# Kernel tuning notes

Measured on AMD Instinct MI355X. Metric: run time of the kernel, lower is better.

Reference implementation:

```python
import jax, jax.numpy as jnp
import numpy as np

D_MODEL = 2048
NUM_Q_HEADS = 16
NUM_KV_HEADS = 4
HEAD_DIM = D_MODEL // NUM_Q_HEADS  # 128
NUM_GROUPS = NUM_Q_HEADS // NUM_KV_HEADS  # 4
ROPE_BASE = 10000.0


def _rope_cos_sin(seq_len, head_dim):
    inv_freq = 1.0 / (ROPE_BASE ** (jnp.arange(0, head_dim, 2, dtype=jnp.float32) / head_dim))
    t = jnp.arange(seq_len, dtype=jnp.float32)
    freqs = jnp.outer(t, inv_freq)            # [S, head_dim/2]
    emb = jnp.concatenate([freqs, freqs], -1)  # [S, head_dim]
    return jnp.cos(emb)[None, :, None, :], jnp.sin(emb)[None, :, None, :]


def _rotate_half(x):
    half = x.shape[-1] // 2
    return jnp.concatenate([-x[..., half:], x[..., :half]], axis=-1)


def setup_inputs() -> dict:
    key = jax.random.key(0)
    k0, k1, k2, k3, k4 = jax.random.split(key, 5)
    B, S = 2, 2048
    kv_dim = HEAD_DIM * NUM_KV_HEADS
    scale = D_MODEL ** -0.5
    return {
        "x": jax.random.normal(k0, (B, S, D_MODEL), jnp.float32),
        "attention_mask": jnp.ones((B, S), jnp.int32),
        "Wq": jax.random.normal(k1, (D_MODEL, D_MODEL), jnp.float32) * scale,
        "Wk": jax.random.normal(k2, (D_MODEL, kv_dim), jnp.float32) * scale,
        "Wv": jax.random.normal(k3, (D_MODEL, kv_dim), jnp.float32) * scale,
        "Wo": jax.random.normal(k4, (D_MODEL, D_MODEL), jnp.float32) * scale,
    }


def reference(x, attention_mask, Wq, Wk, Wv, Wo):
    B, S, _ = x.shape
    q = (x @ Wq).reshape(B, S, NUM_Q_HEADS, HEAD_DIM)
    k = (x @ Wk).reshape(B, S, NUM_KV_HEADS, HEAD_DIM)
    v = (x @ Wv).reshape(B, S, NUM_KV_HEADS, HEAD_DIM)

    cos, sin = _rope_cos_sin(S, HEAD_DIM)  # [1,S,1,hd]
    q = q * cos + _rotate_half(q) * sin
    k = k * cos + _rotate_half(k) * sin

    # [B, H, S, hd]; replicate KV heads across groups (repeat_interleave)
    q = q.transpose(0, 2, 1, 3)
    k = jnp.repeat(k.transpose(0, 2, 1, 3), NUM_GROUPS, axis=1)
    v = jnp.repeat(v.transpose(0, 2, 1, 3), NUM_GROUPS, axis=1)

    scale = HEAD_DIM ** -0.5
    scores = jnp.einsum("bhqd,bhkd->bhqk", q, k) * scale
    mask = attention_mask[:, None, None, :]  # [B,1,1,S] over keys
    scores = jnp.where(mask == 0, jnp.float32(-jnp.inf), scores)
    probs = jax.nn.softmax(scores, axis=-1)
    out = jnp.einsum("bhqk,bhkd->bhqd", probs, v)
    out = out.transpose(0, 2, 1, 3).reshape(B, S, D_MODEL)
    return out @ Wo
```

## Files before the change

### kernel.cpp

```cpp
#include <hip/hip_runtime.h>
#include <hip/hip_bf16.h>

typedef __attribute__((ext_vector_type(4))) float f32x4;
typedef __attribute__((ext_vector_type(16))) float f32x16;
typedef __attribute__((ext_vector_type(8))) short s16x8;
typedef __attribute__((ext_vector_type(4))) short s16x4;
typedef __attribute__((ext_vector_type(2))) unsigned int u32x2;

__device__ __forceinline__ float fexp2(float x) {
    float y; asm("v_exp_f32 %0, %1" : "=v"(y) : "v"(x)); return y;
}

__global__ void tables_prep(float* __restrict__ cosT2, float* __restrict__ sinT2,
                            const int* __restrict__ mask, float* __restrict__ mb) {
    const int bid = blockIdx.x;
    if (bid < 64) {
        const int j = bid;
        const float inv = exp2f(-(float)j * (13.287712379549449f / 64.f));
#pragma unroll
        for (int k = 0; k < 8; ++k) {
            const int s = k * 256 + threadIdx.x;
            const float f = (float)s * inv;
            cosT2[j * 2048 + s] = cosf(f);
            sinT2[j * 2048 + s] = sinf(f);
        }
    } else {
        const int idx = (bid - 64) * 256 + threadIdx.x;
        mb[idx] = (mask[idx] == 0) ? -1e30f : 0.f;
    }
}

__global__ __launch_bounds__(256)
void cast_f32_bf16(const float* __restrict__ src, __hip_bfloat16* __restrict__ dst, int n4) {
    const int i = blockIdx.x * 256 + threadIdx.x;
    if (i < n4) {
        f32x4 v = *reinterpret_cast<const f32x4*>(src + (size_t)i * 4);
        union { s16x4 v4; __hip_bfloat16 h[4]; } u;
#pragma unroll
        for (int j = 0; j < 4; ++j) u.h[j] = __float2bfloat16(v[j]);
        *reinterpret_cast<s16x4*>(dst + (size_t)i * 4) = u.v4;
    }
}

__global__ __launch_bounds__(256)
void transpose_cast_all(const float* __restrict__ Wq, const float* __restrict__ Wk,
                        const float* __restrict__ Wv, const float* __restrict__ Wo,
                        __hip_bfloat16* __restrict__ wqkv_t, __hip_bfloat16* __restrict__ wo_t) {
    __shared__ __align__(16) float t[32][33];
    const int tx = threadIdx.x, ty = threadIdx.y;
    const int xseg = blockIdx.x;
    const int r0 = blockIdx.y * 32;
    const float* src; __hip_bfloat16* dst; int C, c0; bool perm;
    if (xseg < 64)      { src = Wq; dst = wqkv_t;                  C = 2048; c0 = xseg * 32;        perm = true; }
    else if (xseg < 80) { src = Wk; dst = wqkv_t + 2048ULL * 2048; C = 512;  c0 = (xseg - 64) * 32; perm = true; }
    else if (xseg < 96) { src = Wv; dst = wqkv_t + 2560ULL * 2048; C = 512;  c0 = (xseg - 80) * 32; perm = false; }
    else                { src = Wo; dst = wo_t;                    C = 2048; c0 = (xseg - 96) * 32; perm = false; }
#pragma unroll
    for (int i = 0; i < 32; i += 8)
        t[ty + i][tx] = src[(size_t)(r0 + ty + i) * C + c0 + tx];
    __syncthreads();
#pragma unroll
    for (int i = 0; i < 32; i += 8) {
        int row = c0 + ty + i;
        if (perm)
            row = (row & ~127) + (row & 15) + 32 * ((row >> 4) & 3) + 16 * ((row >> 6) & 1);
        dst[(size_t)row * 2048 + r0 + tx] = __float2bfloat16(t[tx][ty + i]);
    }
}

__global__ __launch_bounds__(512, 1)
void gemm_qkv_fused(const __hip_bfloat16* __restrict__ A,
                    const __hip_bfloat16* __restrict__ Bt,
                    const float* __restrict__ cosT2, const float* __restrict__ sinT2,
                    __hip_bfloat16* __restrict__ Qr, __hip_bfloat16* __restrict__ Kr,
                    __hip_bfloat16* __restrict__ Vt, int K) {
    __shared__ __align__(16) __hip_bfloat16 sm[4][2][8192];
    const int tid = threadIdx.x;
    const int l = tid & 63, w = tid >> 6;
    const int lo = l & 15, hi = l >> 4;
    const int wm = w >> 2, wn = w & 3;
    const int id = blockIdx.x, slot = id >> 3;
    const int by = (id & 7) * 2 + slot / 12;
    const int bx = slot % 12;
    const int row0 = by * 256;
    const int col0 = bx * 256;
    const int nk = K >> 5;

    f32x4 acc[8][4];
#pragma unroll
    for (int mi = 0; mi < 8; ++mi)
#pragma unroll
        for (int ni = 0; ni < 4; ++ni) acc[mi][ni] = f32x4{0.f, 0.f, 0.f, 0.f};

    auto ldlds = [&](const __hip_bfloat16* gsrc, __hip_bfloat16* ldst) {
        __builtin_amdgcn_global_load_lds(
            (const __attribute__((address_space(1))) void*)gsrc,
            (__attribute__((address_space(3))) void*)ldst, 16, 0, 0);
    };
    auto stage = [&](int kt) {
        const int s = kt & 3, k0 = kt << 5;
#pragma unroll
        for (int i = 0; i < 2; ++i) {
            const int c = i * 512 + tid;
            const int r = c >> 2, sw = ((c & 3) ^ ((r >> 1) & 3)) * 8;
            ldlds(A + (size_t)(row0 + r) * K + k0 + sw, &sm[s][0][c * 8]);
        }
#pragma unroll
        for (int i = 0; i < 2; ++i) {
            const int c = i * 512 + tid;
            const int r = c >> 2, sw = ((c & 3) ^ ((r >> 1) & 3)) * 8;
            ldlds(Bt + (size_t)(col0 + r) * K + k0 + sw, &sm[s][1][c * 8]);
        }
    };

    stage(0); stage(1); stage(2);
    for (int kt = 0; kt < nk; ++kt) {
        const int s = kt & 3;
        if (kt < nk - 2)       asm volatile("s_waitcnt vmcnt(8)" ::: "memory");
        else if (kt == nk - 2) asm volatile("s_waitcnt vmcnt(4)" ::: "memory");
        else                   asm volatile("s_waitcnt vmcnt(0)" ::: "memory");
        asm volatile("s_waitcnt lgkmcnt(0)" ::: "memory");
        asm volatile("s_barrier" ::: "memory");
        if (kt + 3 < nk) stage(kt + 3);

        s16x8 af[8], bf[4];
        const int rsw = ((lo >> 1) & 3);
#pragma unroll
        for (int mi = 0; mi < 8; ++mi)
            af[mi] = *reinterpret_cast<const s16x8*>(
                &sm[s][0][(wm * 128 + mi * 16 + lo) * 32 + ((hi ^ rsw) * 8)]);
#pragma unroll
        for (int ni = 0; ni < 4; ++ni)
            bf[ni] = *reinterpret_cast<const s16x8*>(
                &sm[s][1][(wn * 64 + ni * 16 + lo) * 32 + ((hi ^ rsw) * 8)]);
        __builtin_amdgcn_s_setprio(1);
#pragma unroll
        for (int mi = 0; mi < 8; ++mi)
#pragma unroll
            for (int ni = 0; ni < 4; ++ni)
                acc[mi][ni] = __builtin_amdgcn_mfma_f32_16x16x32_bf16(af[mi], bf[ni], acc[mi][ni], 0, 0, 0);
        __builtin_amdgcn_s_setprio(0);
    }

    const int rbase = row0 + wm * 128 + hi * 4;
    if (bx < 10) {
        const int cw = col0 + wn * 64;
        const bool isQ = (bx < 8);
        const int head = (isQ ? cw : cw - 2048) >> 7;
        __hip_bfloat16* dst = isQ ? (Qr + ((size_t)head * 2048) * 128)
                                  : (Kr + ((size_t)head * 2048) * 128);
        const size_t bstride = (isQ ? 16ull : 4ull) * 2048 * 128;
        const int jbase = 32 * (wn & 1) + lo;
#pragma unroll
        for (int mi = 0; mi < 8; ++mi) {
            const int tok = rbase + mi * 16;
            const int b = tok >> 11, s0 = tok & 2047;
            __hip_bfloat16* drow = dst + b * bstride + (size_t)s0 * 128;
#pragma unroll
            for (int np = 0; np < 2; ++np) {
                const int j = jbase + 16 * np;
                const f32x4 c4 = *reinterpret_cast<const f32x4*>(cosT2 + j * 2048 + s0);
                const f32x4 s4 = *reinterpret_cast<const f32x4*>(sinT2 + j * 2048 + s0);
                const int ni0 = 2 * np, ni1 = 2 * np + 1;
                const int dd0 = j;
#pragma unroll
                for (int r = 0; r < 4; ++r) {
                    const float v0 = acc[mi][ni0][r], v1 = acc[mi][ni1][r];
                    drow[(size_t)r * 128 + dd0]      = __float2bfloat16(v0 * c4[r] - v1 * s4[r]);
                    drow[(size_t)r * 128 + dd0 + 64] = __float2bfloat16(v1 * c4[r] + v0 * s4[r]);
                }
            }
        }
    } else {
        const int cw = col0 + wn * 64 - 2560;
        const int hh = cw >> 7;
#pragma unroll
        for (int mi = 0; mi < 8; ++mi) {
            const int tok = rbase + mi * 16;
            const int b = tok >> 11, s0 = tok & 2047;
#pragma unroll
            for (int ni = 0; ni < 4; ++ni) {
                const int dd = (cw & 127) + ni * 16 + lo;
                union { s16x4 v4; __hip_bfloat16 h[4]; } u;
#pragma unroll
                for (int r = 0; r < 4; ++r) u.h[r] = __float2bfloat16(acc[mi][ni][r]);
                *reinterpret_cast<s16x4*>(
                    &Vt[((size_t)(b * 4 + hh) * 128 + dd) * 2048 + s0]) = u.v4;
            }
        }
    }
}

template<int NI, bool BF16OUT>
__global__ __launch_bounds__(512, 1)
void gemm256_bt(const __hip_bfloat16* __restrict__ A,
                const __hip_bfloat16* __restrict__ Bt,
                void* __restrict__ Cv, int M, int N, int K, int NX) {
    __shared__ __align__(16) __hip_bfloat16 sm[4][2][8192];
    const int tid = threadIdx.x;
    const int l = tid & 63, w = tid >> 6;
    const int lo = l & 15, hi = l >> 4;
    const int wm = w >> 2, wn = w & 3;
    const int id = blockIdx.x, slot = id >> 3;
    const int by = (id & 7) * 2 + slot / NX;
    const int bx = slot % NX;
    const int row0 = by * 256;
    const int col0 = bx * (NI * 64);
    const int nk = K >> 5;

    f32x4 acc[8][NI];
#pragma unroll
    for (int mi = 0; mi < 8; ++mi)
#pragma unroll
        for (int ni = 0; ni < NI; ++ni) acc[mi][ni] = f32x4{0.f, 0.f, 0.f, 0.f};

    auto ldlds = [&](const __hip_bfloat16* gsrc, __hip_bfloat16* ldst) {
        __builtin_amdgcn_global_load_lds(
            (const __attribute__((address_space(1))) void*)gsrc,
            (__attribute__((address_space(3))) void*)ldst, 16, 0, 0);
    };
    auto stage = [&](int kt) {
        const int s = kt & 3, k0 = kt << 5;
#pragma unroll
        for (int i = 0; i < 2; ++i) {
            const int c = i * 512 + tid;
            const int r = c >> 2, sw = ((c & 3) ^ ((r >> 1) & 3)) * 8;
            ldlds(A + (size_t)(row0 + r) * K + k0 + sw, &sm[s][0][c * 8]);
        }
        {
            const int c = tid;
            const int r = c >> 2, sw = ((c & 3) ^ ((r >> 1) & 3)) * 8;
            ldlds(Bt + (size_t)(col0 + r) * K + k0 + sw, &sm[s][1][c * 8]);
        }
        if constexpr (NI == 4) {
            const int c = 512 + tid;
            const int r = c >> 2, sw = ((c & 3) ^ ((r >> 1) & 3)) * 8;
            ldlds(Bt + (size_t)(col0 + r) * K + k0 + sw, &sm[s][1][c * 8]);
        }
    };

    stage(0); stage(1); stage(2);
    for (int kt = 0; kt < nk; ++kt) {
        const int s = kt & 3;
        if (kt < nk - 2) {
            if constexpr (NI == 4) asm volatile("s_waitcnt vmcnt(8)" ::: "memory");
            else                   asm volatile("s_waitcnt vmcnt(6)" ::: "memory");
        } else if (kt == nk - 2) {
            if constexpr (NI == 4) asm volatile("s_waitcnt vmcnt(4)" ::: "memory");
            else                   asm volatile("s_waitcnt vmcnt(3)" ::: "memory");
        } else {
            asm volatile("s_waitcnt vmcnt(0)" ::: "memory");
        }
        asm volatile("s_waitcnt lgkmcnt(0)" ::: "memory");
        asm volatile("s_barrier" ::: "memory");
        if (kt + 3 < nk) stage(kt + 3);

        s16x8 af[8], bf[NI];
        const int rsw = ((lo >> 1) & 3);
#pragma unroll
        for (int mi = 0; mi < 8; ++mi)
            af[mi] = *reinterpret_cast<const s16x8*>(
                &sm[s][0][(wm * 128 + mi * 16 + lo) * 32 + ((hi ^ rsw) * 8)]);
#pragma unroll
        for (int ni = 0; ni < NI; ++ni)
            bf[ni] = *reinterpret_cast<const s16x8*>(
                &sm[s][1][(wn * NI * 16 + ni * 16 + lo) * 32 + ((hi ^ rsw) * 8)]);
        __builtin_amdgcn_s_setprio(1);
#pragma unroll
        for (int mi = 0; mi < 8; ++mi)
#pragma unroll
            for (int ni = 0; ni < NI; ++ni)
                acc[mi][ni] = __builtin_amdgcn_mfma_f32_16x16x32_bf16(af[mi], bf[ni], acc[mi][ni], 0, 0, 0);
        __builtin_amdgcn_s_setprio(0);
    }
    const int rbase = row0 + wm * 128 + hi * 4;
    const int cbase = col0 + wn * NI * 16 + lo;
    if constexpr (BF16OUT) {
        __hip_bfloat16* C = (__hip_bfloat16*)Cv;
#pragma unroll
        for (int mi = 0; mi < 8; ++mi)
#pragma unroll
            for (int ni = 0; ni < NI; ++ni)
#pragma unroll
                for (int r = 0; r < 4; ++r)
                    C[(size_t)(rbase + mi * 16 + r) * N + cbase + ni * 16] =
                        __float2bfloat16(acc[mi][ni][r]);
    } else {
        float* C = (float*)Cv;
#pragma unroll
        for (int mi = 0; mi < 8; ++mi)
#pragma unroll
            for (int ni = 0; ni < NI; ++ni)
#pragma unroll
                for (int r = 0; r < 4; ++r)
                    C[(size_t)(rbase + mi * 16 + r) * N + cbase + ni * 16] = acc[mi][ni][r];
    }
}

__global__ __launch_bounds__(256, 2)
void attn_kernel(const __hip_bfloat16* __restrict__ Qr,
                 const __hip_bfloat16* __restrict__ Kr,
                 const __hip_bfloat16* __restrict__ Vt,
                 const float* __restrict__ maskb,
                 __hip_bfloat16* __restrict__ Oo) {
    const int S = 2048;
    const int id = blockIdx.x;
    const int v = (id & 7) * 64 + (id >> 3);
    const int qt = v & 15;
    const int bh = v >> 4;
    const int b = bh >> 4, h = bh & 15, kvh = h >> 2;
    const int tid = threadIdx.x;
    const int l = tid & 63, wv_ = tid >> 6;
    const int lq = l & 31, hi2 = l >> 5;
    __shared__ __align__(16) __hip_bfloat16 Ks[2][64 * 128];
    __shared__ __align__(16) __hip_bfloat16 Vs[2][128 * 64];

    const __hip_bfloat16* Qb = Qr + (size_t)(b * 16 + h) * S * 128;
    const __hip_bfloat16* Kb = Kr + (size_t)(b * 4 + kvh) * S * 128;
    const __hip_bfloat16* Vb = Vt + (size_t)(b * 4 + kvh) * 128 * S;
    const float* mrow = maskb + b * S;

    const int qrow = qt * 128 + wv_ * 32 + lq;
    s16x8 qf[8];
#pragma unroll
    for (int ks = 0; ks < 8; ++ks)
        qf[ks] = *reinterpret_cast<const s16x8*>(Qb + (size_t)qrow * 128 + ks * 16 + hi2 * 8);

    float m_run = 0.f, l_run = 0.f;
    f32x16 o[4];
#pragma unroll
    for (int dt = 0; dt < 4; ++dt)
#pragma unroll
        for (int r = 0; r < 16; ++r) o[dt][r] = 0.f;
    const float scale2 = 0.12751682f;

    const int krow = tid >> 4, kc8 = tid & 15;
    const int koff = (kc8 ^ (krow & 7)) * 8;
    const int vrow = tid >> 3, vc8 = tid & 7;
    const int voff = (vc8 ^ (vrow & 7)) * 8;

    s16x8 kreg[4], vreg[4];
    auto load_tile = [&](int kv0) {
#pragma unroll
        for (int i = 0; i < 4; ++i)
            kreg[i] = *reinterpret_cast<const s16x8*>(
                Kb + (size_t)(kv0 + i * 16 + krow) * 128 + kc8 * 8);
#pragma unroll
        for (int i = 0; i < 4; ++i)
            vreg[i] = *reinterpret_cast<const s16x8*>(
                Vb + (size_t)(i * 32 + vrow) * S + kv0 + vc8 * 8);
    };

    auto body = [&](int kt, __hip_bfloat16* Kc, __hip_bfloat16* Vc) {
        const int kv0 = kt * 64;
        f32x4 bi[2][4];
#pragma unroll
        for (int sub = 0; sub < 2; ++sub)
#pragma unroll
            for (int r4 = 0; r4 < 4; ++r4)
                bi[sub][r4] = *reinterpret_cast<const f32x4*>(
                    mrow + kv0 + sub * 32 + r4 * 8 + hi2 * 4);
#pragma unroll
        for (int i = 0; i < 4; ++i)
            *reinterpret_cast<s16x8*>(Kc + (i * 16 + krow) * 128 + koff) = kreg[i];
#pragma unroll
        for (int i = 0; i < 4; ++i)
            *reinterpret_cast<s16x8*>(Vc + (i * 32 + vrow) * 64 + voff) = vreg[i];
        if (kt < 31) load_tile(kv0 + 64);
        asm volatile("s_waitcnt lgkmcnt(0)" ::: "memory");
        asm volatile("s_barrier" ::: "memory");

        f32x16 sc[2];
#pragma unroll
        for (int sub = 0; sub < 2; ++sub)
#pragma unroll
            for (int r = 0; r < 16; ++r) sc[sub][r] = 0.f;
        __builtin_amdgcn_s_setprio(1);
#pragma unroll
        for (int sub = 0; sub < 2; ++sub) {
            const int kr = sub * 32 + lq;
            const int ksw = kr & 7;
#pragma unroll
            for (int ks = 0; ks < 8; ++ks) {
                s16x8 kf = *reinterpret_cast<const s16x8*>(
                    Kc + kr * 128 + (((ks * 2 + hi2) ^ ksw) * 8));
                sc[sub] = __builtin_amdgcn_mfma_f32_32x32x16_bf16(kf, qf[ks], sc[sub], 0, 0, 0);
            }
        }
        __builtin_amdgcn_s_setprio(0);
#pragma unroll
        for (int sub = 0; sub < 2; ++sub)
#pragma unroll
            for (int r = 0; r < 16; ++r)
                sc[sub][r] = fmaf(sc[sub][r], scale2, bi[sub][r >> 2][r & 3]);
        float mx = sc[0][0];
#pragma unroll
        for (int sub = 0; sub < 2; ++sub)
#pragma unroll
            for (int r = 0; r < 16; ++r) mx = fmaxf(mx, sc[sub][r]);
        float ss = 0.f;
#pragma unroll
        for (int sub = 0; sub < 2; ++sub)
#pragma unroll
            for (int r = 0; r < 16; ++r) {
                sc[sub][r] = fexp2(sc[sub][r] - m_run);
                ss += sc[sub][r];
            }
        mx = fmaxf(mx, __shfl_xor(mx, 32));
        if (__ballot(mx > m_run + 11.5417f) != 0ull) {
            const float mnew = fmaxf(m_run, mx);
            const float alpha = fexp2(m_run - mnew);
            m_run = mnew;
            l_run *= alpha;
            ss *= alpha;
#pragma unroll
            for (int sub = 0; sub < 2; ++sub)
#pragma unroll
                for (int r = 0; r < 16; ++r) sc[sub][r] *= alpha;
#pragma unroll
            for (int dt = 0; dt < 4; ++dt)
#pragma unroll
                for (int r = 0; r < 16; ++r) o[dt][r] *= alpha;
        }
        ss += __shfl_xor(ss, 32);
        l_run += ss;
        unsigned int wvp[8][2];
#pragma unroll
        for (int g = 0; g < 8; ++g) {
            const int sub = g >> 2, r4 = g & 3;
            asm("v_cvt_pk_bf16_f32 %0, %1, %2"
                : "=v"(wvp[g][0]) : "v"(sc[sub][r4 * 4 + 0]), "v"(sc[sub][r4 * 4 + 1]));
            asm("v_cvt_pk_bf16_f32 %0, %1, %2"
                : "=v"(wvp[g][1]) : "v"(sc[sub][r4 * 4 + 2]), "v"(sc[sub][r4 * 4 + 3]));
        }
        __builtin_amdgcn_s_setprio(1);
#pragma unroll
        for (int ks = 0; ks < 4; ++ks) {
            u32x2 r0 = __builtin_amdgcn_permlane32_swap(wvp[2 * ks][0], wvp[2 * ks + 1][0], false, false);
            u32x2 r1 = __builtin_amdgcn_permlane32_swap(wvp[2 * ks][1], wvp[2 * ks + 1][1], false, false);
            union { unsigned int u[4]; s16x8 v; } pf;
            pf.u[0] = r0.x; pf.u[1] = r1.x; pf.u[2] = r0.y; pf.u[3] = r1.y;
#pragma unroll
            for (int dt = 0; dt < 4; ++dt) {
                const int dvr = dt * 32 + lq;
                s16x8 vf = *reinterpret_cast<const s16x8*>(
                    Vc + dvr * 64 + (((ks * 2 + hi2) ^ (dvr & 7)) * 8));
                o[dt] = __builtin_amdgcn_mfma_f32_32x32x16_bf16(vf, pf.v, o[dt], 0, 0, 0);
            }
        }
        __builtin_amdgcn_s_setprio(0);
    };

    load_tile(0);
    for (int kt2 = 0; kt2 < 16; ++kt2) {
        body(2 * kt2,     &Ks[0][0], &Vs[0][0]);
        body(2 * kt2 + 1, &Ks[1][0], &Vs[1][0]);
    }
    const float inv = 1.f / l_run;
    const size_t obase = (size_t)(b * S + qt * 128 + wv_ * 32 + lq) * 2048 + h * 128;
#pragma unroll
    for (int dt = 0; dt < 4; ++dt)
#pragma unroll
        for (int r4 = 0; r4 < 4; ++r4) {
            union { s16x4 v4; __hip_bfloat16 hh[4]; } u;
#pragma unroll
            for (int j = 0; j < 4; ++j)
                u.hh[j] = __float2bfloat16(o[dt][r4 * 4 + j] * inv);
            *reinterpret_cast<s16x4*>(&Oo[obase + dt * 32 + r4 * 8 + hi2 * 4]) = u.v4;
        }
}

extern "C" void kernel_launch(void* const* d_in, const int* in_sizes, int n_in,
                              void* d_out, int out_size, void* d_ws, size_t ws_size,
                              hipStream_t stream) {
    const float* x  = (const float*)d_in[0];
    const int* mask = (const int*)d_in[1];
    const float* Wq = (const float*)d_in[2];
    const float* Wk = (const float*)d_in[3];
    const float* Wv = (const float*)d_in[4];
    const float* Wo = (const float*)d_in[5];
    float* out = (float*)d_out;

    char* ws = (char*)d_ws;
    size_t off = 0;
    auto alloc = [&](size_t bytes) -> void* {
        void* p = ws + off;
        off += (bytes + 255) & ~(size_t)255;
        return p;
    };
    __hip_bfloat16* xb     = (__hip_bfloat16*)alloc(4096ULL * 2048 * 2);
    __hip_bfloat16* wqkv_t = (__hip_bfloat16*)alloc(3072ULL * 2048 * 2);
    __hip_bfloat16* wo_t   = (__hip_bfloat16*)alloc(2048ULL * 2048 * 2);
    __hip_bfloat16* Qr     = (__hip_bfloat16*)alloc(2ULL * 16 * 2048 * 128 * 2);
    __hip_bfloat16* Kr     = (__hip_bfloat16*)alloc(2ULL * 4 * 2048 * 128 * 2);
    __hip_bfloat16* Vt     = (__hip_bfloat16*)alloc(2ULL * 4 * 2048 * 128 * 2);
    float*          cosT2  = (float*)alloc(64ULL * 2048 * 4);
    float*          sinT2  = (float*)alloc(64ULL * 2048 * 4);
    float*          maskb  = (float*)alloc(2ULL * 2048 * 4);
    __hip_bfloat16* attno  = (__hip_bfloat16*)alloc(4096ULL * 2048 * 2);

    tables_prep<<<dim3(80), dim3(256), 0, stream>>>(cosT2, sinT2, mask, maskb);
    cast_f32_bf16<<<dim3(8192), dim3(256), 0, stream>>>(x, xb, 2097152);
    transpose_cast_all<<<dim3(160, 64), dim3(32, 8), 0, stream>>>(Wq, Wk, Wv, Wo, wqkv_t, wo_t);

    gemm_qkv_fused<<<dim3(192), dim3(512), 0, stream>>>(xb, wqkv_t, cosT2, sinT2,
                                                        Qr, Kr, Vt, 2048);
    attn_kernel<<<dim3(512), dim3(256), 0, stream>>>(Qr, Kr, Vt, maskb, attno);
    gemm256_bt<2, false><<<dim3(256), dim3(512), 0, stream>>>(attno, wo_t, out, 4096, 2048, 2048, 16);
}
```

Before: 211.3 us.

## Merge prep kernels into one launch and widen K-tile LDS swizzle

Combines the rope-table, mask, x-cast and weight transpose-cast kernels into a single mega_prep launch dispatched by block index, removing two kernel launches and their inter-kernel gaps. The attention kernel's K-tile shared-memory XOR swizzle is widened from 3 to 4 bits (16 chunks per 128-element row) to cut LDS bank conflicts on the MFMA operand reads. The fused prep kernel reserves the transpose's shared-memory buffer for every block, which may lower occupancy for the cast blocks.

```diff
diff --git a/kernel.cpp b/kernel.cpp
--- a/kernel.cpp
+++ b/kernel.cpp
@@ -11,60 +11,56 @@
     float y; asm("v_exp_f32 %0, %1" : "=v"(y) : "v"(x)); return y;
 }
 
-__global__ void tables_prep(float* __restrict__ cosT2, float* __restrict__ sinT2,
-                            const int* __restrict__ mask, float* __restrict__ mb) {
-    const int bid = blockIdx.x;
+__global__ __launch_bounds__(256)
+void mega_prep(const float* __restrict__ x, __hip_bfloat16* __restrict__ xb,
+               const float* __restrict__ Wq, const float* __restrict__ Wk,
+               const float* __restrict__ Wv, const float* __restrict__ Wo,
+               __hip_bfloat16* __restrict__ wqkv_t, __hip_bfloat16* __restrict__ wo_t,
+               float* __restrict__ cosT2, float* __restrict__ sinT2,
+               const int* __restrict__ mask, float* __restrict__ mb) {
+    __shared__ __align__(16) float t[32][33];
+    const int bid = blockIdx.x, tid = threadIdx.x;
     if (bid < 64) {
         const int j = bid;
         const float inv = exp2f(-(float)j * (13.287712379549449f / 64.f));
 #pragma unroll
         for (int k = 0; k < 8; ++k) {
-            const int s = k * 256 + threadIdx.x;
+            const int s = k * 256 + tid;
             const float f = (float)s * inv;
             cosT2[j * 2048 + s] = cosf(f);
             sinT2[j * 2048 + s] = sinf(f);
         }
+    } else if (bid < 80) {
+        const int idx = (bid - 64) * 256 + tid;
+        mb[idx] = (mask[idx] == 0) ? -1e30f : 0.f;
+    } else if (bid < 80 + 8192) {
+        const int i = (bid - 80) * 256 + tid;
+        f32x4 v = *reinterpret_cast<const f32x4*>(x + (size_t)i * 4);
+        union { s16x4 v4; __hip_bfloat16 h[4]; } u;
+#pragma unroll
+        for (int j = 0; j < 4; ++j) u.h[j] = __float2bfloat16(v[j]);
+        *reinterpret_cast<s16x4*>(xb + (size_t)i * 4) = u.v4;
     } else {
-        const int idx = (bid - 64) * 256 + threadIdx.x;
-        mb[idx] = (mask[idx] == 0) ? -1e30f : 0.f;
-    }
-}
-
-__global__ __launch_bounds__(256)
-void cast_f32_bf16(const float* __restrict__ src, __hip_bfloat16* __restrict__ dst, int n4) {
-    const int i = blockIdx.x * 256 + threadIdx.x;
-    if (i < n4) {
-        f32x4 v = *reinterpret_cast<const f32x4*>(src + (size_t)i * 4);
-        union { s16x4 v4; __hip_bfloat16 h[4]; } u;
-#pragma unroll
-        for (int j = 0; j < 4; ++j) u.h[j] = __float2bfloat16(v[j]);
-        *reinterpret_cast<s16x4*>(dst + (size_t)i * 4) = u.v4;
-    }
-}
-
-__global__ __launch_bounds__(256)
-void transpose_cast_all(const float* __restrict__ Wq, const float* __restrict__ Wk,
-                        const float* __restrict__ Wv, const float* __restrict__ Wo,
-                        __hip_bfloat16* __restrict__ wqkv_t, __hip_bfloat16* __restrict__ wo_t) {
-    __shared__ __align__(16) float t[32][33];
-    const int tx = threadIdx.x, ty = threadIdx.y;
-    const int xseg = blockIdx.x;
-    const int r0 = blockIdx.y * 32;
-    const float* src; __hip_bfloat16* dst; int C, c0; bool perm;
-    if (xseg < 64)      { src = Wq; dst = wqkv_t;                  C = 2048; c0 = xseg * 32;        perm = true; }
-    else if (xseg < 80) { src = Wk; dst = wqkv_t + 2048ULL * 2048; C = 512;  c0 = (xseg - 64) * 32; perm = true; }
-    else if (xseg < 96) { src = Wv; dst = wqkv_t + 2560ULL * 2048; C = 512;  c0 = (xseg - 80) * 32; perm = false; }
-    else                { src = Wo; dst = wo_t;                    C = 2048; c0 = (xseg - 96) * 32; perm = false; }
-#pragma unroll
-    for (int i = 0; i < 32; i += 8)
-        t[ty + i][tx] = src[(size_t)(r0 + ty + i) * C + c0 + tx];
-    __syncthreads();
-#pragma unroll
-    for (int i = 0; i < 32; i += 8) {
-        int row = c0 + ty + i;
-        if (perm)
-            row = (row & ~127) + (row & 15) + 32 * ((row >> 4) & 3) + 16 * ((row >> 6) & 1);
-        dst[(size_t)row * 2048 + r0 + tx] = __float2bfloat16(t[tx][ty + i]);
+        const int tt = bid - 8272;
+        const int xseg = tt % 160;
+        const int r0 = (tt / 160) * 32;
+        const int tx = tid & 31, ty = tid >> 5;
+        const float* src; __hip_bfloat16* dst; int C, c0; bool perm;
+        if (xseg < 64)      { src = Wq; dst = wqkv_t;                  C = 2048; c0 = xseg * 32;        perm = true; }
+        else if (xseg < 80) { src = Wk; dst = wqkv_t + 2048ULL * 2048; C = 512;  c0 = (xseg - 64) * 32; perm = true; }
+        else if (xseg < 96) { src = Wv; dst = wqkv_t + 2560ULL * 2048; C = 512;  c0 = (xseg - 80) * 32; perm = false; }
+        else                { src = Wo; dst = wo_t;                    C = 2048; c0 = (xseg - 96) * 32; perm = false; }
+#pragma unroll
+        for (int i = 0; i < 32; i += 8)
+            t[ty + i][tx] = src[(size_t)(r0 + ty + i) * C + c0 + tx];
+        __syncthreads();
+#pragma unroll
+        for (int i = 0; i < 32; i += 8) {
+            int row = c0 + ty + i;
+            if (perm)
+                row = (row & ~127) + (row & 15) + 32 * ((row >> 4) & 3) + 16 * ((row >> 6) & 1);
+            dst[(size_t)row * 2048 + r0 + tx] = __float2bfloat16(t[tx][ty + i]);
+        }
     }
 }
 
@@ -335,7 +331,7 @@
     const float scale2 = 0.12751682f;
 
     const int krow = tid >> 4, kc8 = tid & 15;
-    const int koff = (kc8 ^ (krow & 7)) * 8;
+    const int koff = (kc8 ^ (krow & 15)) * 8;
     const int vrow = tid >> 3, vc8 = tid & 7;
     const int voff = (vc8 ^ (vrow & 7)) * 8;
 
@@ -379,7 +375,7 @@
 #pragma unroll
         for (int sub = 0; sub < 2; ++sub) {
             const int kr = sub * 32 + lq;
-            const int ksw = kr & 7;
+            const int ksw = kr & 15;
 #pragma unroll
             for (int ks = 0; ks < 8; ++ks) {
                 s16x8 kf = *reinterpret_cast<const s16x8*>(
@@ -499,10 +495,9 @@
     float*          maskb  = (float*)alloc(2ULL * 2048 * 4);
     __hip_bfloat16* attno  = (__hip_bfloat16*)alloc(4096ULL * 2048 * 2);
 
-    tables_prep<<<dim3(80), dim3(256), 0, stream>>>(cosT2, sinT2, mask, maskb);
-    cast_f32_bf16<<<dim3(8192), dim3(256), 0, stream>>>(x, xb, 2097152);
-    transpose_cast_all<<<dim3(160, 64), dim3(32, 8), 0, stream>>>(Wq, Wk, Wv, Wo, wqkv_t, wo_t);
-
+    mega_prep<<<dim3(18512), dim3(256), 0, stream>>>(x, xb, Wq, Wk, Wv, Wo,
+                                                     wqkv_t, wo_t, cosT2, sinT2,
+                                                     mask, maskb);
     gemm_qkv_fused<<<dim3(192), dim3(512), 0, stream>>>(xb, wqkv_t, cosT2, sinT2,
                                                         Qr, Kr, Vt, 2048);
     attn_kernel<<<dim3(512), dim3(256), 0, stream>>>(Qr, Kr, Vt, maskb, attno);
```

Result: faster. 204.5 us (-3.2%).
